# Kernel optimization log

Measured on AMD Instinct MI355X. Metric: run time of the kernel, lower is better.

Reference implementation:

```python
import jax, jax.numpy as jnp
import numpy as np

N = 100000   # nodes
E = 600000   # edges (no self loops by construction)
F = 64       # feature_size
H = 2 * F    # hidden_size = 128
G = 32       # graphs in batch
L = N // G   # nodes per graph (equal-size graphs)
NEG_SLOPE = 0.2  # GATConv default leaky_relu slope


def setup_inputs() -> dict:
    key = jax.random.key(0)
    ks = jax.random.split(key, 16)
    x = jax.random.normal(ks[0], (N, F), jnp.float32)
    # edges guaranteed to have no self loops (PyG GAT removes then re-adds them)
    src = jax.random.randint(ks[1], (E,), 0, N)
    off = jax.random.randint(ks[2], (E,), 1, N)
    dst = (src + off) % N
    edge_index = jnp.stack([src, dst]).astype(jnp.int32)
    batch = (jnp.arange(N) // L).astype(jnp.int32)
    sF = 1.0 / np.sqrt(F)
    sH = 1.0 / np.sqrt(H)
    return {
        "x": x, "edge_index": edge_index, "batch": batch,
        "W0": jax.random.normal(ks[3], (F, H), jnp.float32) * sF,
        "b0": jnp.zeros((H,), jnp.float32),
        "Wg": jax.random.normal(ks[4], (H, H), jnp.float32) * sH,
        "att_src": jax.random.normal(ks[5], (H,), jnp.float32) * sH,
        "att_dst": jax.random.normal(ks[6], (H,), jnp.float32) * sH,
        "W1": jax.random.normal(ks[7], (H, H), jnp.float32) * sH,
        "b1": jnp.zeros((H,), jnp.float32),
        "W2": jax.random.normal(ks[8], (H, H), jnp.float32) * sH,
        "b2": jnp.zeros((H,), jnp.float32),
        "Wr": jax.random.normal(ks[9], (H, F), jnp.float32) * sH,
        "br": jnp.zeros((F,), jnp.float32),
    }


def _gcn(x, row, col, w, W, b):
    # PyG GCNConv (normalize=True); edges already include self loops, w holds edge weights.
    xw = x @ W
    deg = jax.ops.segment_sum(w, col, num_segments=N)
    dinv = jnp.where(deg > 0, deg, 1.0) ** -0.5
    dinv = jnp.where(deg > 0, dinv, 0.0)
    norm = dinv[row] * w * dinv[col]                      # [E+N]
    out = jax.ops.segment_sum(xw[row] * norm[:, None], col, num_segments=N)
    return out + b


def reference(x, edge_index, batch, W0, b0, Wg, att_src, att_dst, W1, b1, W2, b2, Wr, br):
    row, col = edge_index[0], edge_index[1]
    loops = jnp.arange(N, dtype=edge_index.dtype)
    row_f = jnp.concatenate([row, loops])                 # [E+N] with self loops
    col_f = jnp.concatenate([col, loops])

    # initial GCNConv (gcn_norm adds self loops with weight 1) + relu
    x = jax.nn.relu(_gcn(x, row_f, col_f, jnp.ones(E + N, x.dtype), W0, b0))

    # GATConv attention (heads=1); node output is discarded in the torch module
    xg = x @ Wg
    a_s = xg @ att_src
    a_d = xg @ att_dst
    e = jax.nn.leaky_relu(a_s[row_f] + a_d[col_f], NEG_SLOPE)
    m = jax.ops.segment_max(e, col_f, num_segments=N)
    ex = jnp.exp(e - m[col_f])
    alpha = ex / jax.ops.segment_sum(ex, col_f, num_segments=N)[col_f]

    # gcn_norm's add_remaining_self_loops replaces self-loop weights with 1.0
    w = alpha.at[E:].set(1.0)

    x = jax.nn.relu(_gcn(x, row_f, col_f, w, W1, b1))
    x = jax.nn.relu(_gcn(x, row_f, col_f, w, W2, b2))

    # readout: Dropout (eval -> identity) + Linear
    out = x @ Wr + br                                     # [N, F]

    # unbatch + pad_sequence (batch_first=True); batch ids are sorted
    counts = jax.ops.segment_sum(jnp.ones(N, jnp.int32), batch, num_segments=G)
    starts = jnp.concatenate([jnp.zeros(1, jnp.int32), jnp.cumsum(counts)[:-1].astype(jnp.int32)])
    pos = jnp.arange(N, dtype=jnp.int32) - starts[batch]
    emb = jnp.zeros((G, L, F), out.dtype).at[batch, pos].set(out)
    return emb
```

## Files before the change

### kernel.cpp

```cpp
#include <hip/hip_runtime.h>
#include <hip/hip_bf16.h>
#include <hip/hip_fp16.h>
#include <math.h>

#define NN 100000
#define EE 600000
#define FF 64
#define HH 128
#define CHUNK 1024
#define NCHUNK ((NN + CHUNK - 1) / CHUNK)
#define NCHUNKS_M (NN / 16)
#define PREP_ITEMS (NN * FF / 4 + 49280)

typedef unsigned short u16;
typedef unsigned int u32;
typedef __attribute__((ext_vector_type(8))) short bf16x8;
typedef __attribute__((ext_vector_type(4))) float f32x4;

__device__ __forceinline__ u16 f2bf(float f) {
    __hip_bfloat16 h = __float2bfloat16(f);
    return *(u16*)&h;
}
__device__ __forceinline__ float bf2f(u16 u) {
    unsigned int t = ((unsigned int)u) << 16;
    return *(float*)&t;
}
__device__ __forceinline__ u32 enc_meta(int r, float w) {
    u16 hb = __half_as_ushort(__float2half(w));
    return ((u32)r << 15) | (hb & 0x7fffu);
}
__device__ __forceinline__ void dec_meta(u32 u, int& r, float& w) {
    r = (int)(u >> 15);
    w = __half2float(__ushort_as_half((u16)(u & 0x7fffu)));
}


__global__ void build_k(const int* __restrict__ col, int* __restrict__ cnt,
                        const float* __restrict__ W0, const float* __restrict__ W1,
                        const float* __restrict__ W2, const float* __restrict__ Wr,
                        const float* __restrict__ Wg, const float* __restrict__ att_src,
                        const float* __restrict__ att_dst, const float* __restrict__ x,
                        u16* __restrict__ Wt0, u16* __restrict__ Wt1,
                        u16* __restrict__ Wt2, u16* __restrict__ Wtr,
                        float* __restrict__ vs, float* __restrict__ vd,
                        u16* __restrict__ xb) {
    int i = blockIdx.x * 256 + threadIdx.x;
    if (i < EE) {
        atomicAdd(&cnt[col[i]], 1);
        return;
    }
    i -= EE;
    if (i < NN * FF / 4) {
        float4 v = ((const float4*)x)[i];
        ushort4 o;
        o.x = f2bf(v.x); o.y = f2bf(v.y); o.z = f2bf(v.z); o.w = f2bf(v.w);
        ((ushort4*)xb)[i] = o;
        return;
    }
    i -= NN * FF / 4;
    if (i < 8192) {
        int n = i >> 6, k = i & 63;
        Wt0[i] = f2bf(W0[k * 128 + n]);
        return;
    }
    i -= 8192;
    if (i < 16384) {
        int n = i >> 7, k = i & 127;
        Wt1[i] = f2bf(W1[k * 128 + n]);
        return;
    }
    i -= 16384;
    if (i < 16384) {
        int n = i >> 7, k = i & 127;
        Wt2[i] = f2bf(W2[k * 128 + n]);
        return;
    }
    i -= 16384;
    if (i < 8192) {
        int n = i >> 7, k = i & 127;
        Wtr[i] = f2bf(Wr[k * 64 + n]);
        return;
    }
    i -= 8192;
    if (i < HH) {
        float s1 = 0.f, s2 = 0.f;
        for (int j = 0; j < HH; j++) {
            float w = Wg[i * HH + j];
            s1 += w * att_src[j];
            s2 += w * att_dst[j];
        }
        vs[i] = s1;
        vd[i] = s2;
    }
}

__global__ void chunksum_k(const int* __restrict__ cnt, int* __restrict__ chunk_sum,
                           float* __restrict__ dinv1) {
    int b = blockIdx.x, t = threadIdx.x;
    int base = b * CHUNK + t * 4;
    int s = 0;
    #pragma unroll
    for (int i = 0; i < 4; i++) {
        int idx = base + i;
        if (idx < NN) {
            int cv = cnt[idx];
            s += cv;
            dinv1[idx] = rsqrtf((float)cv + 1.0f);
        }
    }
    __shared__ int sm[4];
    for (int d = 32; d > 0; d >>= 1) s += __shfl_down(s, d);
    if ((t & 63) == 0) sm[t >> 6] = s;
    __syncthreads();
    if (t == 0) chunk_sum[b] = sm[0] + sm[1] + sm[2] + sm[3];
}

__global__ void chunkoff_k(const int* __restrict__ chunk_sum, int* __restrict__ chunk_off,
                           int* __restrict__ col_ptr) {
    if (threadIdx.x == 0) {
        int run = 0;
        for (int i = 0; i < NCHUNK; i++) { chunk_off[i] = run; run += chunk_sum[i]; }
        col_ptr[NN] = run;
    }
}

__global__ void colptr_k(const int* __restrict__ cnt, const int* __restrict__ chunk_off,
                         int* __restrict__ col_ptr, int* __restrict__ cursor) {
    int b = blockIdx.x, t = threadIdx.x;
    int base = b * CHUNK + t * 4;
    int c[4]; int tot = 0;
    #pragma unroll
    for (int i = 0; i < 4; i++) { int idx = base + i; c[i] = (idx < NN) ? cnt[idx] : 0; tot += c[i]; }
    __shared__ int s[256];
    s[t] = tot;
    __syncthreads();
    for (int d = 1; d < 256; d <<= 1) {
        int v = (t >= d) ? s[t - d] : 0;
        __syncthreads();
        s[t] += v;
        __syncthreads();
    }
    int excl = s[t] - tot;
    int off = chunk_off[b] + excl;
    int pre = 0;
    #pragma unroll
    for (int i = 0; i < 4; i++) {
        int idx = base + i;
        if (idx < NN) {
            col_ptr[idx] = off + pre;
            cursor[idx] = off + pre;
        }
        pre += c[i];
    }
}

__global__ void fill_k(const int* __restrict__ row, const int* __restrict__ col,
                       int* __restrict__ cursor, const float* __restrict__ dinv1,
                       u32* __restrict__ meta1) {
    int e = blockIdx.x * 256 + threadIdx.x;
    if (e < EE) {
        int r = row[e], c = col[e];
        int slot = atomicAdd(&cursor[c], 1);
        meta1[slot] = enc_meta(r, dinv1[r] * dinv1[c]);
    }
}


__global__ __launch_bounds__(256, 8) void aggx_k(
    const u16* __restrict__ xb, const int* __restrict__ col_ptr, const u32* __restrict__ meta1,
    const float* __restrict__ dinv1, u16* __restrict__ xout) {
    int wid = threadIdx.x >> 6, lane = threadIdx.x & 63;
    int sub = lane >> 5;
    int c = blockIdx.x * 8 + wid * 2 + sub;
    int hl = lane & 31;
    int g = hl >> 3;
    int ch = (hl & 7) << 3;
    int beg = col_ptr[c], end = col_ptr[c + 1];
    float acc[8] = {};

    int pA = beg + g, pB = pA + 4;
    int rA = 0, rB = 0; float wA = 0.f, wB = 0.f;
    if (pA < end) dec_meta(meta1[pA], rA, wA);
    if (pB < end) dec_meta(meta1[pB], rB, wB);
    while (pA < end) {
        bool hb = pB < end;
        bf16x8 vA = *(const bf16x8*)&xb[(size_t)rA * FF + ch];
        bf16x8 vB;
        if (hb) vB = *(const bf16x8*)&xb[(size_t)rB * FF + ch];
        int pA2 = pA + 8, pB2 = pB + 8;
        int rA2 = 0, rB2 = 0; float wA2 = 0.f, wB2 = 0.f;
        if (pA2 < end) dec_meta(meta1[pA2], rA2, wA2);
        if (pB2 < end) dec_meta(meta1[pB2], rB2, wB2);
        #pragma unroll
        for (int j = 0; j < 8; j++) acc[j] = fmaf(bf2f((u16)vA[j]), wA, acc[j]);
        if (hb) {
            #pragma unroll
            for (int j = 0; j < 8; j++) acc[j] = fmaf(bf2f((u16)vB[j]), wB, acc[j]);
        }
        pA = pA2; pB = pB2; rA = rA2; rB = rB2; wA = wA2; wB = wB2;
    }
    #pragma unroll
    for (int j = 0; j < 8; j++) {
        acc[j] += __shfl_xor(acc[j], 8);
        acc[j] += __shfl_xor(acc[j], 16);
    }

    if (g == 0) {
        bf16x8 v = *(const bf16x8*)&xb[(size_t)c * FF + ch];
        float dc = dinv1[c];
        float ws = dc * dc;
        bf16x8 o;
        #pragma unroll
        for (int j = 0; j < 8; j++) {
            float t = fmaf(bf2f((u16)v[j]), ws, acc[j]);
            o[j] = (short)f2bf(t);
        }
        *(bf16x8*)&xout[(size_t)c * FF + ch] = o;
    }
}


__global__ __launch_bounds__(256) void gemm1_k(const u16* __restrict__ A,
                                               const u16* __restrict__ Wt0,
                                               const u16* __restrict__ Wt1,
                                               const float* __restrict__ bias,
                                               const float* __restrict__ vs, const float* __restrict__ vd,
                                               u16* __restrict__ Y, float* __restrict__ a_s,
                                               float* __restrict__ a_d) {
    constexpr int K = FF, N = HH, KK = K / 32, NT = N / 16, KK2 = HH / 32;
    constexpr int LSTRIDE = 136;
    __shared__ u16 lds[4][16 * LSTRIDE];
    int lane = threadIdx.x & 63, wid = threadIdx.x >> 6;
    int l15 = lane & 15, l4 = lane >> 4;
    int wg = blockIdx.x * 4 + wid;
    int nwaves = gridDim.x * 4;
    u16* myl = &lds[wid][0];

    bf16x8 a_frag[KK][NT];
    #pragma unroll
    for (int kk = 0; kk < KK; kk++)
        #pragma unroll
        for (int nt = 0; nt < NT; nt++)
            a_frag[kk][nt] = *(const bf16x8*)&Wt0[(size_t)(nt * 16 + l15) * K + kk * 32 + l4 * 8];

    for (int ch = wg; ch < NCHUNKS_M; ch += nwaves) {
        int row = ch * 16 + l15;
        bf16x8 b_frag[KK];
        #pragma unroll
        for (int kk = 0; kk < KK; kk++)
            b_frag[kk] = *(const bf16x8*)&A[(size_t)row * K + kk * 32 + l4 * 8];
        f32x4 acc[NT] = {};
        #pragma unroll
        for (int kk = 0; kk < KK; kk++)
            #pragma unroll
            for (int nt = 0; nt < NT; nt++)
                acc[nt] = __builtin_amdgcn_mfma_f32_16x16x32_bf16(a_frag[kk][nt], b_frag[kk],
                                                                  acc[nt], 0, 0, 0);
        float s1 = 0.f, s2 = 0.f;
        #pragma unroll
        for (int nt = 0; nt < NT; nt++) {
            f32x4 b4 = *(const f32x4*)&bias[nt * 16 + l4 * 4];
            f32x4 v4 = *(const f32x4*)&vs[nt * 16 + l4 * 4];
            f32x4 d4 = *(const f32x4*)&vd[nt * 16 + l4 * 4];
            float o0 = fmaxf(acc[nt][0] + b4[0], 0.f);
            float o1 = fmaxf(acc[nt][1] + b4[1], 0.f);
            float o2 = fmaxf(acc[nt][2] + b4[2], 0.f);
            float o3 = fmaxf(acc[nt][3] + b4[3], 0.f);
            ushort4 o;
            o.x = f2bf(o0); o.y = f2bf(o1); o.z = f2bf(o2); o.w = f2bf(o3);
            *(ushort4*)&myl[l15 * LSTRIDE + nt * 16 + l4 * 4] = o;
            s1 += o0 * v4[0] + o1 * v4[1] + o2 * v4[2] + o3 * v4[3];
            s2 += o0 * d4[0] + o1 * d4[1] + o2 * d4[2] + o3 * d4[3];
        }
        s1 += __shfl_xor(s1, 16); s1 += __shfl_xor(s1, 32);
        s2 += __shfl_xor(s2, 16); s2 += __shfl_xor(s2, 32);
        if (l4 == 0) {
            a_s[row] = s1;
            a_d[row] = s2;
        }
        bf16x8 b2[KK2];
        #pragma unroll
        for (int kk2 = 0; kk2 < KK2; kk2++)
            b2[kk2] = *(const bf16x8*)&myl[l15 * LSTRIDE + kk2 * 32 + l4 * 8];
        f32x4 acc2[NT] = {};
        #pragma unroll
        for (int kk2 = 0; kk2 < KK2; kk2++)
            #pragma unroll
            for (int nt = 0; nt < NT; nt++) {
                bf16x8 w1f = *(const bf16x8*)&Wt1[(size_t)(nt * 16 + l15) * HH + kk2 * 32 + l4 * 8];
                acc2[nt] = __builtin_amdgcn_mfma_f32_16x16x32_bf16(w1f, b2[kk2], acc2[nt], 0, 0, 0);
            }
        #pragma unroll
        for (int nt = 0; nt < NT; nt++) {
            ushort4 o;
            o.x = f2bf(acc2[nt][0]);
            o.y = f2bf(acc2[nt][1]);
            o.z = f2bf(acc2[nt][2]);
            o.w = f2bf(acc2[nt][3]);
            *(ushort4*)&Y[(size_t)row * HH + nt * 16 + l4 * 4] = o;
        }
    }
}


template <int K, int N, bool OUTF32>
__global__ __launch_bounds__(256) void mfma_gemm_k(const u16* __restrict__ A,
                                                   const u16* __restrict__ Wt,
                                                   const float* __restrict__ bias,
                                                   void* __restrict__ C_) {
    constexpr int KK = K / 32;
    constexpr int NT = N / 16;
    int lane = threadIdx.x & 63;
    int l15 = lane & 15, l4 = lane >> 4;
    int wg = blockIdx.x * 4 + (threadIdx.x >> 6);
    int nwaves = gridDim.x * 4;

    bf16x8 a_frag[KK][NT];
    #pragma unroll
    for (int kk = 0; kk < KK; kk++)
        #pragma unroll
        for (int nt = 0; nt < NT; nt++)
            a_frag[kk][nt] = *(const bf16x8*)&Wt[(size_t)(nt * 16 + l15) * K + kk * 32 + l4 * 8];

    f32x4 bias_f[NT];
    if (OUTF32) {
        #pragma unroll
        for (int nt = 0; nt < NT; nt++)
            bias_f[nt] = *(const f32x4*)&bias[nt * 16 + l4 * 4];
    }

    float* Cf = (float*)C_;
    u16* Cb = (u16*)C_;

    for (int ch = wg; ch < NCHUNKS_M; ch += nwaves) {
        int row = ch * 16 + l15;
        bf16x8 b_frag[KK];
        #pragma unroll
        for (int kk = 0; kk < KK; kk++)
            b_frag[kk] = *(const bf16x8*)&A[(size_t)row * K + kk * 32 + l4 * 8];
        f32x4 acc[NT] = {};
        #pragma unroll
        for (int kk = 0; kk < KK; kk++)
            #pragma unroll
            for (int nt = 0; nt < NT; nt++)
                acc[nt] = __builtin_amdgcn_mfma_f32_16x16x32_bf16(a_frag[kk][nt], b_frag[kk],
                                                                  acc[nt], 0, 0, 0);
        #pragma unroll
        for (int nt = 0; nt < NT; nt++) {
            int col = nt * 16 + l4 * 4;
            if (OUTF32) {
                float4 o;
                o.x = acc[nt][0] + bias_f[nt][0];
                o.y = acc[nt][1] + bias_f[nt][1];
                o.z = acc[nt][2] + bias_f[nt][2];
                o.w = acc[nt][3] + bias_f[nt][3];
                *(float4*)&Cf[(size_t)row * N + col] = o;
            } else {
                ushort4 o;
                o.x = f2bf(acc[nt][0]);
                o.y = f2bf(acc[nt][1]);
                o.z = f2bf(acc[nt][2]);
                o.w = f2bf(acc[nt][3]);
                *(ushort4*)&Cb[(size_t)row * N + col] = o;
            }
        }
    }
}


__global__ __launch_bounds__(256) void attn_k(const int* __restrict__ col_ptr,
                                              const u32* __restrict__ meta1,
                                              const float* __restrict__ a_s,
                                              const float* __restrict__ a_d,
                                              float* __restrict__ alpha,
                                              float* __restrict__ dinv2) {
    int lane = threadIdx.x & 63, wid = threadIdx.x >> 6;
    int grp = lane >> 3, idx = lane & 7;
    int c = blockIdx.x * 32 + wid * 8 + grp;
    if (c >= NN) return;
    int beg = col_ptr[c], end = col_ptr[c + 1];
    float ad = a_d[c];
    float es = a_s[c] + ad;
    es = (es > 0.f) ? es : 0.2f * es;
    float m = (idx == 0) ? es : -1e30f;
    float s = (idx == 0) ? 1.f : 0.f;
    for (int p = beg + idx; p < end; p += 8) {
        float e = a_s[meta1[p] >> 15] + ad;
        e = (e > 0.f) ? e : 0.2f * e;
        alpha[p] = e;
        float mn = fmaxf(m, e);
        s = s * expf(m - mn) + expf(e - mn);
        m = mn;
    }
    #pragma unroll
    for (int d = 1; d < 8; d <<= 1) {
        float mo = __shfl_xor(m, d);
        float so = __shfl_xor(s, d);
        float mn = fmaxf(m, mo);
        s = s * expf(m - mn) + so * expf(mo - mn);
        m = mn;
    }
    float inv = 1.f / s;
    float aself = expf(es - m) * inv;
    float d2 = rsqrtf(2.f - aself);
    if (idx == 0) dinv2[c] = d2;
    float sc = inv * d2;
    for (int p = beg + idx; p < end; p += 8)
        alpha[p] = expf(alpha[p] - m) * sc;
}

__global__ void w2_k(const u32* __restrict__ meta1, const float* __restrict__ dinv2,
                     const float* __restrict__ alpha, u32* __restrict__ meta2) {
    int p = blockIdx.x * 256 + threadIdx.x;
    if (p < EE) {
        u32 u = meta1[p];
        int r = (int)(u >> 15);
        float w = alpha[p] * dinv2[r];
        u16 hb = __half_as_ushort(__float2half(w));
        meta2[p] = (u & 0xffff8000u) | (hb & 0x7fffu);
    }
}


__global__ __launch_bounds__(256, 8) void agg2_k(
    const u16* __restrict__ xw, const int* __restrict__ col_ptr, const u32* __restrict__ meta2,
    const float* __restrict__ dinv2, const float* __restrict__ bias, u16* __restrict__ xout) {
    int wid = threadIdx.x >> 6, lane = threadIdx.x & 63;
    int sub = lane >> 5;
    int c = blockIdx.x * 8 + wid * 2 + sub;
    int hl = lane & 31;
    int g = hl >> 4;
    int ch = (hl & 15) << 3;
    int beg = col_ptr[c], end = col_ptr[c + 1];
    float acc[8] = {};

    int pA = beg + g, pB = pA + 2, pC = pA + 4;
    int rA = 0, rB = 0, rC = 0; float wA = 0.f, wB = 0.f, wC = 0.f;
    if (pA < end) dec_meta(meta2[pA], rA, wA);
    if (pB < end) dec_meta(meta2[pB], rB, wB);
    if (pC < end) dec_meta(meta2[pC], rC, wC);
    while (pA < end) {
        bool hb = pB < end, hc = pC < end;
        bf16x8 vA = *(const bf16x8*)&xw[(size_t)rA * HH + ch];
        bf16x8 vB, vC;
        if (hb) vB = *(const bf16x8*)&xw[(size_t)rB * HH + ch];
        if (hc) vC = *(const bf16x8*)&xw[(size_t)rC * HH + ch];
        int pA2 = pA + 6, pB2 = pB + 6, pC2 = pC + 6;
        int rA2 = 0, rB2 = 0, rC2 = 0; float wA2 = 0.f, wB2 = 0.f, wC2 = 0.f;
        if (pA2 < end) dec_meta(meta2[pA2], rA2, wA2);
        if (pB2 < end) dec_meta(meta2[pB2], rB2, wB2);
        if (pC2 < end) dec_meta(meta2[pC2], rC2, wC2);
        #pragma unroll
        for (int j = 0; j < 8; j++) acc[j] = fmaf(bf2f((u16)vA[j]), wA, acc[j]);
        if (hb) {
            #pragma unroll
            for (int j = 0; j < 8; j++) acc[j] = fmaf(bf2f((u16)vB[j]), wB, acc[j]);
        }
        if (hc) {
            #pragma unroll
            for (int j = 0; j < 8; j++) acc[j] = fmaf(bf2f((u16)vC[j]), wC, acc[j]);
        }
        pA = pA2; pB = pB2; pC = pC2;
        rA = rA2; rB = rB2; rC = rC2;
        wA = wA2; wB = wB2; wC = wC2;
    }
    #pragma unroll
    for (int j = 0; j < 8; j++) acc[j] += __shfl_xor(acc[j], 16);

    if (g == 0) {
        bf16x8 v = *(const bf16x8*)&xw[(size_t)c * HH + ch];
        float dc = dinv2[c];
        float ws = dc * dc;
        f32x4 b4a = *(const f32x4*)&bias[ch];
        f32x4 b4b = *(const f32x4*)&bias[ch + 4];
        bf16x8 o;
        #pragma unroll
        for (int j = 0; j < 8; j++) {
            float bj = (j < 4) ? b4a[j] : b4b[j - 4];
            float t = fmaxf(fmaf(bf2f((u16)v[j]), ws, acc[j]) + bj, 0.f);
            o[j] = (short)f2bf(t);
        }
        *(bf16x8*)&xout[(size_t)c * HH + ch] = o;
    }
}


extern "C" void kernel_launch(void* const* d_in, const int* in_sizes, int n_in,
                              void* d_out, int out_size, void* d_ws, size_t ws_size,
                              hipStream_t stream) {
    const float* x = (const float*)d_in[0];
    const int* eidx = (const int*)d_in[1];
    const float* W0 = (const float*)d_in[3];
    const float* b0 = (const float*)d_in[4];
    const float* Wg = (const float*)d_in[5];
    const float* att_src = (const float*)d_in[6];
    const float* att_dst = (const float*)d_in[7];
    const float* W1 = (const float*)d_in[8];
    const float* b1 = (const float*)d_in[9];
    const float* W2 = (const float*)d_in[10];
    const float* b2 = (const float*)d_in[11];
    const float* Wr = (const float*)d_in[12];
    const float* br = (const float*)d_in[13];
    float* out = (float*)d_out;

    const int* erow = eidx;
    const int* ecol = eidx + EE;

    char* p = (char*)d_ws;
    auto alloc = [&](size_t bytes) {
        void* r = (void*)p;
        p += (bytes + 255) & ~(size_t)255;
        return r;
    };
    int* col_ptr = (int*)alloc((NN + 1) * sizeof(int));
    u32* meta1 = (u32*)alloc(EE * sizeof(u32));
    u32* meta2 = (u32*)alloc(EE * sizeof(u32));
    int* cnt = (int*)alloc(NN * sizeof(int));
    int* cursor = (int*)alloc(NN * sizeof(int));
    int* chunk_sum = (int*)alloc(128 * sizeof(int));
    int* chunk_off = (int*)alloc(128 * sizeof(int));
    float* alpha = (float*)alloc(EE * sizeof(float));
    float* dinv1 = (float*)alloc(NN * sizeof(float));
    float* dinv2 = (float*)alloc(NN * sizeof(float));
    float* a_s = (float*)alloc(NN * sizeof(float));
    float* a_d = (float*)alloc(NN * sizeof(float));
    float* vs = (float*)alloc(HH * sizeof(float));
    float* vd = (float*)alloc(HH * sizeof(float));
    u16* Wt0 = (u16*)alloc(8192 * sizeof(u16));
    u16* Wt1 = (u16*)alloc(16384 * sizeof(u16));
    u16* Wt2 = (u16*)alloc(16384 * sizeof(u16));
    u16* Wtr = (u16*)alloc(8192 * sizeof(u16));
    u16* xb = (u16*)alloc((size_t)NN * FF * sizeof(u16));
    u16* xaggb = (u16*)alloc((size_t)NN * FF * sizeof(u16));
    u16* bufA = (u16*)alloc((size_t)NN * HH * sizeof(u16));
    u16* bufB = (u16*)alloc((size_t)NN * HH * sizeof(u16));

    hipMemsetAsync(cnt, 0, NN * sizeof(int), stream);

    build_k<<<(EE + PREP_ITEMS + 255) / 256, 256, 0, stream>>>(
        ecol, cnt, W0, W1, W2, Wr, Wg, att_src, att_dst, x,
        Wt0, Wt1, Wt2, Wtr, vs, vd, xb);
    chunksum_k<<<NCHUNK, 256, 0, stream>>>(cnt, chunk_sum, dinv1);
    chunkoff_k<<<1, 64, 0, stream>>>(chunk_sum, chunk_off, col_ptr);
    colptr_k<<<NCHUNK, 256, 0, stream>>>(cnt, chunk_off, col_ptr, cursor);
    fill_k<<<(EE + 255) / 256, 256, 0, stream>>>(erow, ecol, cursor, dinv1, meta1);

    int aggGrid = NN / 8;
    const int GG = 512;

    aggx_k<<<aggGrid, 256, 0, stream>>>(xb, col_ptr, meta1, dinv1, xaggb);
    gemm1_k<<<GG, 256, 0, stream>>>(xaggb, Wt0, Wt1, b0, vs, vd, bufB, a_s, a_d);
    attn_k<<<(NN + 31) / 32, 256, 0, stream>>>(col_ptr, meta1, a_s, a_d, alpha, dinv2);
    w2_k<<<(EE + 255) / 256, 256, 0, stream>>>(meta1, dinv2, alpha, meta2);
    agg2_k<<<aggGrid, 256, 0, stream>>>(bufB, col_ptr, meta2, dinv2, b1, bufA);
    mfma_gemm_k<HH, HH, false><<<GG, 256, 0, stream>>>(bufA, Wt2, nullptr, bufB);
    agg2_k<<<aggGrid, 256, 0, stream>>>(bufB, col_ptr, meta2, dinv2, b2, bufA);
    mfma_gemm_k<HH, FF, true><<<GG, 256, 0, stream>>>(bufA, Wtr, br, out);
}
```

Before: 242.2 us.

## Fuse GCN aggregation with following GEMM and fold chunk offsets into colptr

Merges each agg2 aggregation kernel with the following dense MFMA GEMM: a block aggregates 16 nodes into LDS, then four waves multiply that tile by the next weight matrix and write the projected output directly. This removes a full N x 128 bf16 intermediate write and read per layer and two launches. Aggregation now uses 16 threads per node with no edge split, so there is less memory-level parallelism per node. The single-thread chunkoff kernel is also removed: each colptr block serially sums the preceding chunk sums, and col_ptr[NN] is hardcoded to EE.

```diff
diff --git a/kernel.cpp b/kernel.cpp
--- a/kernel.cpp
+++ b/kernel.cpp
@@ -115,18 +115,16 @@
     if (t == 0) chunk_sum[b] = sm[0] + sm[1] + sm[2] + sm[3];
 }
 
-__global__ void chunkoff_k(const int* __restrict__ chunk_sum, int* __restrict__ chunk_off,
-                           int* __restrict__ col_ptr) {
-    if (threadIdx.x == 0) {
-        int run = 0;
-        for (int i = 0; i < NCHUNK; i++) { chunk_off[i] = run; run += chunk_sum[i]; }
-        col_ptr[NN] = run;
-    }
-}
-
-__global__ void colptr_k(const int* __restrict__ cnt, const int* __restrict__ chunk_off,
+__global__ void colptr_k(const int* __restrict__ cnt, const int* __restrict__ chunk_sum,
                          int* __restrict__ col_ptr, int* __restrict__ cursor) {
     int b = blockIdx.x, t = threadIdx.x;
+    __shared__ int base_off;
+    if (t == 0) {
+        int run = 0;
+        for (int i = 0; i < b; i++) run += chunk_sum[i];
+        base_off = run;
+        if (b == 0) col_ptr[NN] = EE;
+    }
     int base = b * CHUNK + t * 4;
     int c[4]; int tot = 0;
     #pragma unroll
@@ -141,7 +139,7 @@
         __syncthreads();
     }
     int excl = s[t] - tot;
-    int off = chunk_off[b] + excl;
+    int off = base_off + excl;
     int pre = 0;
     #pragma unroll
     for (int i = 0; i < 4; i++) {
@@ -298,71 +296,6 @@
             o.z = f2bf(acc2[nt][2]);
             o.w = f2bf(acc2[nt][3]);
             *(ushort4*)&Y[(size_t)row * HH + nt * 16 + l4 * 4] = o;
-        }
-    }
-}
-
-
-template <int K, int N, bool OUTF32>
-__global__ __launch_bounds__(256) void mfma_gemm_k(const u16* __restrict__ A,
-                                                   const u16* __restrict__ Wt,
-                                                   const float* __restrict__ bias,
-                                                   void* __restrict__ C_) {
-    constexpr int KK = K / 32;
-    constexpr int NT = N / 16;
-    int lane = threadIdx.x & 63;
-    int l15 = lane & 15, l4 = lane >> 4;
-    int wg = blockIdx.x * 4 + (threadIdx.x >> 6);
-    int nwaves = gridDim.x * 4;
-
-    bf16x8 a_frag[KK][NT];
-    #pragma unroll
-    for (int kk = 0; kk < KK; kk++)
-        #pragma unroll
-        for (int nt = 0; nt < NT; nt++)
-            a_frag[kk][nt] = *(const bf16x8*)&Wt[(size_t)(nt * 16 + l15) * K + kk * 32 + l4 * 8];
-
-    f32x4 bias_f[NT];
-    if (OUTF32) {
-        #pragma unroll
-        for (int nt = 0; nt < NT; nt++)
-            bias_f[nt] = *(const f32x4*)&bias[nt * 16 + l4 * 4];
-    }
-
-    float* Cf = (float*)C_;
-    u16* Cb = (u16*)C_;
-
-    for (int ch = wg; ch < NCHUNKS_M; ch += nwaves) {
-        int row = ch * 16 + l15;
-        bf16x8 b_frag[KK];
-        #pragma unroll
-        for (int kk = 0; kk < KK; kk++)
-            b_frag[kk] = *(const bf16x8*)&A[(size_t)row * K + kk * 32 + l4 * 8];
-        f32x4 acc[NT] = {};
-        #pragma unroll
-        for (int kk = 0; kk < KK; kk++)
-            #pragma unroll
-            for (int nt = 0; nt < NT; nt++)
-                acc[nt] = __builtin_amdgcn_mfma_f32_16x16x32_bf16(a_frag[kk][nt], b_frag[kk],
-                                                                  acc[nt], 0, 0, 0);
-        #pragma unroll
-        for (int nt = 0; nt < NT; nt++) {
-            int col = nt * 16 + l4 * 4;
-            if (OUTF32) {
-                float4 o;
-                o.x = acc[nt][0] + bias_f[nt][0];
-                o.y = acc[nt][1] + bias_f[nt][1];
-                o.z = acc[nt][2] + bias_f[nt][2];
-                o.w = acc[nt][3] + bias_f[nt][3];
-                *(float4*)&Cf[(size_t)row * N + col] = o;
-            } else {
-                ushort4 o;
-                o.x = f2bf(acc[nt][0]);
-                o.y = f2bf(acc[nt][1]);
-                o.z = f2bf(acc[nt][2]);
-                o.w = f2bf(acc[nt][3]);
-                *(ushort4*)&Cb[(size_t)row * N + col] = o;
-            }
         }
     }
 }
@@ -422,34 +355,41 @@
 }
 
 
-__global__ __launch_bounds__(256, 8) void agg2_k(
-    const u16* __restrict__ xw, const int* __restrict__ col_ptr, const u32* __restrict__ meta2,
-    const float* __restrict__ dinv2, const float* __restrict__ bias, u16* __restrict__ xout) {
-    int wid = threadIdx.x >> 6, lane = threadIdx.x & 63;
-    int sub = lane >> 5;
-    int c = blockIdx.x * 8 + wid * 2 + sub;
-    int hl = lane & 31;
-    int g = hl >> 4;
-    int ch = (hl & 15) << 3;
+template <int NOUT, bool OUTF32>
+__global__ __launch_bounds__(256, 8) void agg_gemm_k(
+    const u16* __restrict__ xw, const int* __restrict__ col_ptr, const u32* __restrict__ meta,
+    const float* __restrict__ dinv2, const float* __restrict__ bias_in,
+    const u16* __restrict__ Wt, const float* __restrict__ bias_out, void* __restrict__ Y_) {
+    constexpr int KK2 = HH / 32;
+    constexpr int NT = NOUT / 16;
+    constexpr int NT_W = NT / 4;
+    constexpr int LSTRIDE = 136;
+    __shared__ u16 lds[16 * LSTRIDE];
+    int tid = threadIdx.x;
+    int lane = tid & 63, wid = tid >> 6;
+    int node = tid >> 4;
+    int ch = (tid & 15) << 3;
+    int cbase = blockIdx.x * 16;
+    int c = cbase + node;
     int beg = col_ptr[c], end = col_ptr[c + 1];
     float acc[8] = {};
 
-    int pA = beg + g, pB = pA + 2, pC = pA + 4;
+    int pA = beg, pB = beg + 1, pC = beg + 2;
     int rA = 0, rB = 0, rC = 0; float wA = 0.f, wB = 0.f, wC = 0.f;
-    if (pA < end) dec_meta(meta2[pA], rA, wA);
-    if (pB < end) dec_meta(meta2[pB], rB, wB);
-    if (pC < end) dec_meta(meta2[pC], rC, wC);
+    if (pA < end) dec_meta(meta[pA], rA, wA);
+    if (pB < end) dec_meta(meta[pB], rB, wB);
+    if (pC < end) dec_meta(meta[pC], rC, wC);
     while (pA < end) {
         bool hb = pB < end, hc = pC < end;
         bf16x8 vA = *(const bf16x8*)&xw[(size_t)rA * HH + ch];
         bf16x8 vB, vC;
         if (hb) vB = *(const bf16x8*)&xw[(size_t)rB * HH + ch];
         if (hc) vC = *(const bf16x8*)&xw[(size_t)rC * HH + ch];
-        int pA2 = pA + 6, pB2 = pB + 6, pC2 = pC + 6;
+        int pA2 = pA + 3, pB2 = pB + 3, pC2 = pC + 3;
         int rA2 = 0, rB2 = 0, rC2 = 0; float wA2 = 0.f, wB2 = 0.f, wC2 = 0.f;
-        if (pA2 < end) dec_meta(meta2[pA2], rA2, wA2);
-        if (pB2 < end) dec_meta(meta2[pB2], rB2, wB2);
-        if (pC2 < end) dec_meta(meta2[pC2], rC2, wC2);
+        if (pA2 < end) dec_meta(meta[pA2], rA2, wA2);
+        if (pB2 < end) dec_meta(meta[pB2], rB2, wB2);
+        if (pC2 < end) dec_meta(meta[pC2], rC2, wC2);
         #pragma unroll
         for (int j = 0; j < 8; j++) acc[j] = fmaf(bf2f((u16)vA[j]), wA, acc[j]);
         if (hb) {
@@ -464,15 +404,12 @@
         rA = rA2; rB = rB2; rC = rC2;
         wA = wA2; wB = wB2; wC = wC2;
     }
-    #pragma unroll
-    for (int j = 0; j < 8; j++) acc[j] += __shfl_xor(acc[j], 16);
-
-    if (g == 0) {
+    {
         bf16x8 v = *(const bf16x8*)&xw[(size_t)c * HH + ch];
         float dc = dinv2[c];
         float ws = dc * dc;
-        f32x4 b4a = *(const f32x4*)&bias[ch];
-        f32x4 b4b = *(const f32x4*)&bias[ch + 4];
+        f32x4 b4a = *(const f32x4*)&bias_in[ch];
+        f32x4 b4b = *(const f32x4*)&bias_in[ch + 4];
         bf16x8 o;
         #pragma unroll
         for (int j = 0; j < 8; j++) {
@@ -480,7 +417,42 @@
             float t = fmaxf(fmaf(bf2f((u16)v[j]), ws, acc[j]) + bj, 0.f);
             o[j] = (short)f2bf(t);
         }
-        *(bf16x8*)&xout[(size_t)c * HH + ch] = o;
+        *(bf16x8*)&lds[node * LSTRIDE + ch] = o;
+    }
+    __syncthreads();
+
+    int l15 = lane & 15, l4 = lane >> 4;
+    bf16x8 b2[KK2];
+    #pragma unroll
+    for (int kk2 = 0; kk2 < KK2; kk2++)
+        b2[kk2] = *(const bf16x8*)&lds[l15 * LSTRIDE + kk2 * 32 + l4 * 8];
+    int row = cbase + l15;
+    #pragma unroll
+    for (int ntw = 0; ntw < NT_W; ntw++) {
+        int nt = wid * NT_W + ntw;
+        f32x4 acc2 = {};
+        #pragma unroll
+        for (int kk2 = 0; kk2 < KK2; kk2++) {
+            bf16x8 wf = *(const bf16x8*)&Wt[(size_t)(nt * 16 + l15) * HH + kk2 * 32 + l4 * 8];
+            acc2 = __builtin_amdgcn_mfma_f32_16x16x32_bf16(wf, b2[kk2], acc2, 0, 0, 0);
+        }
+        int col = nt * 16 + l4 * 4;
+        if (OUTF32) {
+            float4 o;
+            f32x4 bo = *(const f32x4*)&bias_out[col];
+            o.x = acc2[0] + bo[0];
+            o.y = acc2[1] + bo[1];
+            o.z = acc2[2] + bo[2];
+            o.w = acc2[3] + bo[3];
+            *(float4*)&((float*)Y_)[(size_t)row * NOUT + col] = o;
+        } else {
+            ushort4 o;
+            o.x = f2bf(acc2[0]);
+            o.y = f2bf(acc2[1]);
+            o.z = f2bf(acc2[2]);
+            o.w = f2bf(acc2[3]);
+            *(ushort4*)&((u16*)Y_)[(size_t)row * NOUT + col] = o;
+        }
     }
 }
 
@@ -518,7 +490,6 @@
     int* cnt = (int*)alloc(NN * sizeof(int));
     int* cursor = (int*)alloc(NN * sizeof(int));
     int* chunk_sum = (int*)alloc(128 * sizeof(int));
-    int* chunk_off = (int*)alloc(128 * sizeof(int));
     float* alpha = (float*)alloc(EE * sizeof(float));
     float* dinv1 = (float*)alloc(NN * sizeof(float));
     float* dinv2 = (float*)alloc(NN * sizeof(float));
@@ -541,8 +512,7 @@
         ecol, cnt, W0, W1, W2, Wr, Wg, att_src, att_dst, x,
         Wt0, Wt1, Wt2, Wtr, vs, vd, xb);
     chunksum_k<<<NCHUNK, 256, 0, stream>>>(cnt, chunk_sum, dinv1);
-    chunkoff_k<<<1, 64, 0, stream>>>(chunk_sum, chunk_off, col_ptr);
-    colptr_k<<<NCHUNK, 256, 0, stream>>>(cnt, chunk_off, col_ptr, cursor);
+    colptr_k<<<NCHUNK, 256, 0, stream>>>(cnt, chunk_sum, col_ptr, cursor);
     fill_k<<<(EE + 255) / 256, 256, 0, stream>>>(erow, ecol, cursor, dinv1, meta1);
 
     int aggGrid = NN / 8;
@@ -552,8 +522,8 @@
     gemm1_k<<<GG, 256, 0, stream>>>(xaggb, Wt0, Wt1, b0, vs, vd, bufB, a_s, a_d);
     attn_k<<<(NN + 31) / 32, 256, 0, stream>>>(col_ptr, meta1, a_s, a_d, alpha, dinv2);
     w2_k<<<(EE + 255) / 256, 256, 0, stream>>>(meta1, dinv2, alpha, meta2);
-    agg2_k<<<aggGrid, 256, 0, stream>>>(bufB, col_ptr, meta2, dinv2, b1, bufA);
-    mfma_gemm_k<HH, HH, false><<<GG, 256, 0, stream>>>(bufA, Wt2, nullptr, bufB);
-    agg2_k<<<aggGrid, 256, 0, stream>>>(bufB, col_ptr, meta2, dinv2, b2, bufA);
-    mfma_gemm_k<HH, FF, true><<<GG, 256, 0, stream>>>(bufA, Wtr, br, out);
-}
+    agg_gemm_k<HH, false><<<NCHUNKS_M, 256, 0, stream>>>(bufB, col_ptr, meta2, dinv2, b1,
+                                                         Wt2, nullptr, bufA);
+    agg_gemm_k<FF, true><<<NCHUNKS_M, 256, 0, stream>>>(bufA, col_ptr, meta2, dinv2, b2,
+                                                        Wtr, br, out);
+}
```

Result: faster. 236.5 us (-2.4%).
